# Optimization experiments

Measured on AMD Instinct MI355X. Metric: run time of the kernel, lower is better.

The kernel has to match this reference:

```python
import jax, jax.numpy as jnp
import numpy as np

B = 16      # number of graphs (equal-sized, batch = repeat(arange(B), N))


def _knn_edges(pos, k, total):
    """Batch-aware kNN graph, torch_geometric knn_graph semantics.

    loop=False, flow='source_to_target': for each query node i, its k nearest
    neighbors j produce edges (row=j neighbor/source, col=i query/target).
    Returns (row, col) as flat global int32 index arrays of length B*N*k.
    """
    N = total // B
    posb = pos.reshape(B, N, -1)                      # [B, N, 3]
    sq = jnp.sum(posb * posb, axis=-1)                # [B, N]
    # squared Euclidean distances, [B, N, N]
    d2 = sq[:, :, None] + sq[:, None, :] - 2.0 * jnp.einsum('bnd,bmd->bnm', posb, posb)
    d2 = jnp.where(jnp.eye(N, dtype=bool)[None], jnp.inf, d2)  # exclude self-loops
    _, nbr = jax.lax.top_k(-d2, k)                    # [B, N, k] local neighbor idx
    offs = (jnp.arange(B, dtype=nbr.dtype) * N)[:, None, None]
    row = (nbr + offs).reshape(-1)                                      # neighbors (sources)
    col = jnp.broadcast_to(jnp.arange(N, dtype=nbr.dtype)[None, :, None] + offs,
                           (B, N, k)).reshape(-1)                       # query nodes (targets)
    return row, col


def reference(x, pos, batch, k):
    total = x.shape[0]
    row, col = _knn_edges(pos, k, total)
    # scatter_mean(x[col], row, dim_size=total): mean of gathered features per row index
    sums = jax.ops.segment_sum(x[col], row, num_segments=total)          # [total, d]
    cnt = jax.ops.segment_sum(jnp.ones(row.shape, x.dtype), row, num_segments=total)
    x_neigh_mean = sums / jnp.maximum(cnt, 1.0)[:, None]                 # empty rows -> 0
    return jnp.sum(jnp.abs(x - x_neigh_mean), axis=-1)                   # L1 norm, [total]


def setup_inputs() -> dict:
    key = jax.random.key(0)
    k1, k2 = jax.random.split(key)
    N = 4096
    x = jax.random.normal(k1, (B * N, 64), dtype=jnp.float32)
    pos = jax.random.normal(k2, (B * N, 3), dtype=jnp.float32)
    batch = jnp.repeat(jnp.arange(B, dtype=jnp.int64), N)
    return {"x": x, "pos": pos, "batch": batch, "k": 10}
```

## Files before the change

kernel.cpp:

```cpp
#include <hip/hip_runtime.h>
#include <stdint.h>

#define NB 16
#define NN 4096
#define KK 10
#define NL 8
#define NSEL 11
#define LPITCH 9
#define FD 64
#define TOTAL (NB * NN)
#define NW 8
#define CH 512
#define QG 64
#define WCAP 24
#define WPITCH 25
#define SLOTP 11

#define INFF __int_as_float(0x7f800000)

typedef float f2 __attribute__((ext_vector_type(2)));

__device__ __forceinline__ f2 FdP3(f2 cx, f2 cy, f2 cz, f2 cq,
                                   f2 vx2, f2 vy2, f2 vz2) {
#pragma clang fp contract(fast)
    f2 t = vx2 * cx + cq;
    t = vy2 * cy + t;
    t = vz2 * cz + t;
    return t;
}

__device__ __forceinline__ uint32_t d2exact(float mx, float my, float mz, float sqi,
                                            float cx, float cy, float cz, float cw) {
    float dot = __fadd_rn(__fadd_rn(__fmul_rn(mx, cx), __fmul_rn(my, cy)),
                          __fmul_rn(mz, cz));
    float d2 = __fsub_rn(__fadd_rn(sqi, cw), __fmul_rn(2.0f, dot));
    return __float_as_uint(d2);
}

__global__ __launch_bounds__(256) void prep_kernel(const float* __restrict__ pos,
                                                   float4* __restrict__ pp4,
                                                   int* __restrict__ cnt) {
    const int p = blockIdx.x * 256 + threadIdx.x;
    const float* s = pos + (size_t)p * 6;
    float x0 = s[0], y0 = s[1], z0 = s[2];
    float x1 = s[3], y1 = s[4], z1 = s[5];
    float q0 = __fadd_rn(__fadd_rn(__fmul_rn(x0, x0), __fmul_rn(y0, y0)),
                         __fmul_rn(z0, z0));
    float q1 = __fadd_rn(__fadd_rn(__fmul_rn(x1, x1), __fmul_rn(y1, y1)),
                         __fmul_rn(z1, z1));
    pp4[2 * p + 0] = make_float4(x0, x1, y0, y1);
    pp4[2 * p + 1] = make_float4(z0, z1, q0, q1);
    cnt[2 * p + 0] = 0;
    cnt[2 * p + 1] = 0;
}

__global__ __launch_bounds__(512, 8) void knn_kernel(const float4* __restrict__ pp4,
                                                     int* __restrict__ cnt,
                                                     int* __restrict__ colfix,
                                                     int* __restrict__ nbr) {
    __shared__ uint64_t smem8[3200];
    __shared__ float tau_s[QG];
    float* listf = (float*)smem8;
    uint16_t* pool16 = (uint16_t*)smem8;
    uint64_t* slot = smem8;

    const int tid = threadIdx.x;
    const int lane = tid & 63;
    const int w = __builtin_amdgcn_readfirstlane(tid >> 6);
    const int batch = blockIdx.x & 15;
    const int qloc = ((blockIdx.x >> 4) << 6) | lane;
    const int gbase = batch << 12;
    const int gq = gbase + qloc;

    float4 mA = pp4[(gq >> 1) * 2 + 0];
    float4 mB = pp4[(gq >> 1) * 2 + 1];
    const bool hi = (qloc & 1);
    const float mx = hi ? mA.y : mA.x;
    const float my = hi ? mA.w : mA.z;
    const float mz = hi ? mB.y : mB.x;
    const float sqi = hi ? mB.w : mB.z;
    const f2 vx22 = {__fmul_rn(-2.0f, mx), __fmul_rn(-2.0f, mx)};
    const f2 vy22 = {__fmul_rn(-2.0f, my), __fmul_rn(-2.0f, my)};
    const f2 vz22 = {__fmul_rn(-2.0f, mz), __fmul_rn(-2.0f, mz)};

    const f2* __restrict__ cp2 = (const f2*)(pp4 + (size_t)(gbase + w * CH));

#define D8P(cb2)                                                      \
    f2 X0 = (cb2)[0],  Y0 = (cb2)[1],  Z0 = (cb2)[2],  Q0 = (cb2)[3]; \
    f2 X1 = (cb2)[4],  Y1 = (cb2)[5],  Z1 = (cb2)[6],  Q1 = (cb2)[7]; \
    f2 X2 = (cb2)[8],  Y2 = (cb2)[9],  Z2 = (cb2)[10], Q2 = (cb2)[11];\
    f2 X3 = (cb2)[12], Y3 = (cb2)[13], Z3 = (cb2)[14], Q3 = (cb2)[15];\
    f2 e0 = FdP3(X0, Y0, Z0, Q0, vx22, vy22, vz22);                   \
    f2 e1 = FdP3(X1, Y1, Z1, Q1, vx22, vy22, vz22);                   \
    f2 e2 = FdP3(X2, Y2, Z2, Q2, vx22, vy22, vz22);                   \
    f2 e3 = FdP3(X3, Y3, Z3, Q3, vx22, vy22, vz22);

    float L[NL];
#pragma unroll
    for (int t = 0; t < NL; t++) L[t] = INFF;

#pragma unroll 2
    for (int g = 0; g < NL; ++g) {
        float gm = INFF;
#pragma unroll
        for (int s = 0; s < 4; ++s) {
            const f2* cb2 = cp2 + (g * 4 + s) * 16;
            D8P(cb2);
            float m = fminf(fminf(fminf(e0.x, e0.y), fminf(e1.x, e1.y)),
                            fminf(fminf(e2.x, e2.y), fminf(e3.x, e3.y)));
            gm = fminf(gm, m);
        }
#pragma unroll
        for (int t = 0; t < NL - 1; ++t) L[t] = __builtin_amdgcn_fmed3f(L[t], L[t + 1], gm);
        L[NL - 1] = fminf(L[NL - 1], gm);
    }
#pragma unroll
    for (int t = 0; t < NL; t++) listf[tid * LPITCH + t] = L[t];
    __syncthreads();

    if (tid < QG) {
        int p[NW];
#pragma unroll
        for (int u = 0; u < NW; u++) p[u] = NL - 1;
        float tau = INFF;
        for (int it = 0; it < NSEL; ++it) {
            float best = INFF;
            int bw = 0;
#pragma unroll
            for (int u = 0; u < NW; u++) {
                float v = (p[u] >= 0) ? listf[((u << 6) | tid) * LPITCH + p[u]] : INFF;
                if (v < best) { best = v; bw = u; }
            }
            p[bw]--;
            tau = best;
        }
        tau_s[tid] = tau;
    }
    __syncthreads();

    const float t0v = tau_s[lane];
    const float tau = t0v + fabsf(t0v) * 1e-4f + 1e-4f;
    const uint32_t cell0 = (uint32_t)(((w << 6) | lane) * WPITCH);
    uint32_t cpos = cell0;
#pragma unroll 2
    for (int o = 0; o < CH / 8; ++o) {
        const f2* cb2 = cp2 + o * 16;
        D8P(cb2);
        const uint32_t jb = (uint32_t)(w * CH + o * 8);
        bool h0 = e0.x <= tau, h1 = e0.y <= tau, h2 = e1.x <= tau, h3 = e1.y <= tau;
        bool h4 = e2.x <= tau, h5 = e2.y <= tau, h6 = e3.x <= tau, h7 = e3.y <= tau;
#define PUSH(hv, off)                                              \
        if ((hv) && cpos < cell0 + WCAP) {                         \
            pool16[cpos] = (uint16_t)(jb + (off));                 \
            cpos++;                                                \
        }
        if (h0 | h1) { PUSH(h0, 0) PUSH(h1, 1) }
        if (h2 | h3) { PUSH(h2, 2) PUSH(h3, 3) }
        if (h4 | h5) { PUSH(h4, 4) PUSH(h5, 5) }
        if (h6 | h7) { PUSH(h6, 6) PUSH(h7, 7) }
#undef PUSH
    }

    uint64_t S[KK];
#pragma unroll
    for (int t = 0; t < KK; t++) S[t] = ~0ull;
    {
        const uint16_t* st = pool16 + cell0;
        const int c2i = (int)(cpos - cell0);
        for (int e = 0; e < c2i; ++e) {
            uint32_t ix = st[e];
            if (ix == (uint32_t)qloc) continue;
            int g = gbase + (int)ix;
            float4 A4 = pp4[(g >> 1) * 2 + 0];
            float4 B4 = pp4[(g >> 1) * 2 + 1];
            bool ch = (ix & 1);
            uint32_t db = d2exact(mx, my, mz, sqi,
                                  ch ? A4.y : A4.x, ch ? A4.w : A4.z,
                                  ch ? B4.y : B4.x, ch ? B4.w : B4.z);
            uint64_t k64 = ((uint64_t)db << 32) | ix;
            if (k64 < S[0]) {
                bool sh[KK];
                sh[0] = true;
#pragma unroll
                for (int t = 1; t < KK; t++) sh[t] = (k64 < S[t]);
#pragma unroll
                for (int t = 0; t < KK; t++) {
                    uint64_t vac = sh[t] ? k64 : S[t];
                    S[t] = (t + 1 < KK) ? (sh[t + 1] ? S[t + 1] : vac) : vac;
                }
            }
        }
    }
    __syncthreads();

    if (w >= 4) {
        uint64_t* sl = slot + (((w - 4) << 6) | lane) * SLOTP;
#pragma unroll
        for (int j = 0; j < KK; ++j) sl[j] = S[KK - 1 - j];
    }
    __syncthreads();

    if (w < 4) {
        uint64_t* sl = slot + ((w << 6) | lane) * SLOTP;
        uint64_t P[KK];
#pragma unroll
        for (int j = 0; j < KK; ++j) P[j] = sl[j];
#pragma unroll
        for (int j = 0; j < KK; ++j) {
            uint64_t v = S[KK - 1 - j];
            uint32_t r = (uint32_t)j;
#pragma unroll
            for (int i = 0; i < KK; ++i) r += (P[i] < v) ? 1u : 0u;
            if (r < KK) sl[r] = v;
        }
#pragma unroll
        for (int i = 0; i < KK; ++i) {
            uint64_t v = P[i];
            uint32_t r = (uint32_t)i;
#pragma unroll
            for (int t = 0; t < KK; ++t) r += (S[t] <= v) ? 1u : 0u;
            if (r < KK) sl[r] = v;
        }
    }
    __syncthreads();

    if (w < 2) {
        uint64_t* sa = slot + (((w * 2) << 6) | lane) * SLOTP;
        uint64_t* sb = slot + (((w * 2 + 1) << 6) | lane) * SLOTP;
        uint64_t Aa[KK], Bb[KK];
#pragma unroll
        for (int j = 0; j < KK; ++j) Aa[j] = sa[j];
#pragma unroll
        for (int j = 0; j < KK; ++j) Bb[j] = sb[j];
#pragma unroll
        for (int j = 0; j < KK; ++j) {
            uint32_t r = (uint32_t)j;
#pragma unroll
            for (int i = 0; i < KK; ++i) r += (Bb[i] < Aa[j]) ? 1u : 0u;
            if (r < KK) sa[r] = Aa[j];
        }
#pragma unroll
        for (int i = 0; i < KK; ++i) {
            uint32_t r = (uint32_t)i;
#pragma unroll
            for (int j = 0; j < KK; ++j) r += (Aa[j] <= Bb[i]) ? 1u : 0u;
            if (r < KK) sa[r] = Bb[i];
        }
    }
    __syncthreads();

    if (tid < QG) {
        const uint64_t* sa = slot + ((0 << 6) | tid) * SLOTP;
        const uint64_t* sb = slot + ((2 << 6) | tid) * SLOTP;
        uint64_t Aa[KK], Bb[KK];
#pragma unroll
        for (int j = 0; j < KK; ++j) Aa[j] = sa[j];
#pragma unroll
        for (int j = 0; j < KK; ++j) Bb[j] = sb[j];
#define EMIT(key, rk)                                              \
        {                                                          \
            int jl = (int)((key) & 0xffffffffu);                   \
            int gj = gbase + jl;                                   \
            int p = atomicAdd(&cnt[gj], 1);                        \
            if (colfix) {                                          \
                if (p < 64) colfix[(gj << 6) | p] = gq;            \
            } else {                                               \
                nbr[gq * KK + (int)(rk)] = gj;                     \
            }                                                      \
        }
#pragma unroll
        for (int j = 0; j < KK; ++j) {
            uint32_t r = (uint32_t)j;
#pragma unroll
            for (int i = 0; i < KK; ++i) r += (Bb[i] < Aa[j]) ? 1u : 0u;
            if (r < KK) EMIT(Aa[j], r)
        }
#pragma unroll
        for (int i = 0; i < KK; ++i) {
            uint32_t r = (uint32_t)i;
#pragma unroll
            for (int j = 0; j < KK; ++j) r += (Aa[j] <= Bb[i]) ? 1u : 0u;
            if (r < KK) EMIT(Bb[i], r)
        }
#undef EMIT
    }
#undef D8P
}

__global__ __launch_bounds__(256) void out_bucket_kernel(const float4* __restrict__ x4,
                                                         const int* __restrict__ colfix,
                                                         const int* __restrict__ cnt,
                                                         float* __restrict__ out) {
    const int b = blockIdx.x;
    const int g = b & 15;
    const int i = b >> 4;
    const int l = threadIdx.x & 31;
    const int n = (g << 12) | (i << 3) | (threadIdx.x >> 5);
    const int s = l & 15;
    const int half = l >> 4;
    const int c = cnt[n];
    const int cc = (c > 64) ? 64 : c;
    const int4* cf4 = (const int4*)(colfix + ((size_t)n << 6));
    float4 acc = make_float4(0.f, 0.f, 0.f, 0.f);
    for (int eb = half * 4; eb < cc; eb += 8) {
        int4 Q = cf4[eb >> 2];
        float4 v0 = x4[((size_t)Q.x << 4) | s];
        acc.x += v0.x; acc.y += v0.y; acc.z += v0.z; acc.w += v0.w;
        if (eb + 1 < cc) {
            float4 v1 = x4[((size_t)Q.y << 4) | s];
            acc.x += v1.x; acc.y += v1.y; acc.z += v1.z; acc.w += v1.w;
        }
        if (eb + 2 < cc) {
            float4 v2 = x4[((size_t)Q.z << 4) | s];
            acc.x += v2.x; acc.y += v2.y; acc.z += v2.z; acc.w += v2.w;
        }
        if (eb + 3 < cc) {
            float4 v3 = x4[((size_t)Q.w << 4) | s];
            acc.x += v3.x; acc.y += v3.y; acc.z += v3.z; acc.w += v3.w;
        }
    }
    acc.x += __shfl_xor(acc.x, 16, 64);
    acc.y += __shfl_xor(acc.y, 16, 64);
    acc.z += __shfl_xor(acc.z, 16, 64);
    acc.w += __shfl_xor(acc.w, 16, 64);
    const float inv = 1.0f / (float)(c > 1 ? c : 1);
    float4 mn = x4[((size_t)n << 4) | s];
    float v = fabsf(mn.x - acc.x * inv) + fabsf(mn.y - acc.y * inv) +
              fabsf(mn.z - acc.z * inv) + fabsf(mn.w - acc.w * inv);
    v += __shfl_xor(v, 1, 64);
    v += __shfl_xor(v, 2, 64);
    v += __shfl_xor(v, 4, 64);
    v += __shfl_xor(v, 8, 64);
    if (l == 0) out[n] = v;
}

__global__ __launch_bounds__(1024) void scan_kernel(const int* __restrict__ cnt,
                                                    int* __restrict__ offs) {
    __shared__ int lds[1024];
    const int t = threadIdx.x;
    const int base = t * 64;
    int s = 0;
    for (int i = 0; i < 64; i++) s += cnt[base + i];
    lds[t] = s;
    __syncthreads();
    for (int off = 1; off < 1024; off <<= 1) {
        int v = (t >= off) ? lds[t - off] : 0;
        __syncthreads();
        lds[t] += v;
        __syncthreads();
    }
    int run = lds[t] - s;
    for (int i = 0; i < 64; i++) {
        offs[base + i] = run;
        run += cnt[base + i];
    }
}

__global__ __launch_bounds__(256) void fill_kernel(const int* __restrict__ nbr,
                                                   int* __restrict__ offs,
                                                   int* __restrict__ col) {
    const int i = blockIdx.x * 256 + threadIdx.x;
#pragma unroll
    for (int t = 0; t < KK; t++) {
        int j = nbr[i * KK + t];
        int p = atomicAdd(&offs[j], 1);
        col[p] = i;
    }
}

__global__ __launch_bounds__(256) void out_kernel(const float* __restrict__ x,
                                                  const int* __restrict__ col,
                                                  const int* __restrict__ offs_end,
                                                  const int* __restrict__ cnt,
                                                  float* __restrict__ out) {
    const int gtid = blockIdx.x * 256 + threadIdx.x;
    const int n = gtid >> 6;
    const int lane = gtid & 63;
    const int c = cnt[n];
    const int end = offs_end[n];
    const int start = end - c;
    float s = 0.0f;
    for (int e = start; e < end; e++) {
        int i = col[e];
        s += x[(size_t)i * FD + lane];
    }
    float mean = s / (float)(c > 1 ? c : 1);
    float v = fabsf(x[(size_t)n * FD + lane] - mean);
#pragma unroll
    for (int off = 32; off; off >>= 1) v += __shfl_xor(v, off, 64);
    if (lane == 0) out[n] = v;
}

extern "C" void kernel_launch(void* const* d_in, const int* in_sizes, int n_in,
                              void* d_out, int out_size, void* d_ws, size_t ws_size,
                              hipStream_t stream) {
    const float* x = (const float*)d_in[0];
    const float* pos = (const float*)d_in[1];
    float* out = (float*)d_out;

    char* ws = (char*)d_ws;
    float4* pp4 = (float4*)(ws + 0);
    int* cnt = (int*)(ws + 1048576);
    int* colfix = (int*)(ws + 1310720);
    int* nbr = (int*)(ws + 1310720);
    int* offs = (int*)(ws + 3932160);
    int* col = (int*)(ws + 4194304);

    const bool bucket = ws_size >= (size_t)(1310720 + TOTAL * 64 * 4);

    hipLaunchKernelGGL(prep_kernel, dim3(TOTAL / 2 / 256), dim3(256), 0, stream, pos, pp4, cnt);
    hipLaunchKernelGGL(knn_kernel, dim3(TOTAL / QG), dim3(512), 0, stream, pp4, cnt,
                       bucket ? colfix : (int*)nullptr, bucket ? (int*)nullptr : nbr);
    if (bucket) {
        hipLaunchKernelGGL(out_bucket_kernel, dim3(TOTAL * 32 / 256), dim3(256), 0, stream,
                           (const float4*)x, colfix, cnt, out);
    } else {
        hipLaunchKernelGGL(scan_kernel, dim3(1), dim3(1024), 0, stream, cnt, offs);
        hipLaunchKernelGGL(fill_kernel, dim3(TOTAL / 256), dim3(256), 0, stream, nbr, offs, col);
        hipLaunchKernelGGL(out_kernel, dim3(TOTAL * FD / 256), dim3(256), 0, stream,
                           x, col, offs, cnt, out);
    }
}
```

Measured before the change: 175.0 us.

## Sort points by Morton grid cell and prune kNN candidates with group bounding boxes

After: 188.3 us. 7.6% more time.

```diff
diff --git a/kernel.cpp b/kernel.cpp
--- a/kernel.cpp
+++ b/kernel.cpp
@@ -5,6 +5,8 @@
 #define NN 4096
 #define KK 10
 #define NL 8
+#define NL2 11
+#define LP2 11
 #define NSEL 11
 #define LPITCH 9
 #define FD 64
@@ -14,7 +16,15 @@
 #define QG 64
 #define WCAP 24
 #define WPITCH 25
+#define QCAP 192
 #define SLOTP 11
+#define GSZ 32
+#define NGRP (TOTAL / GSZ)
+
+#define OFF_HIST 18087936
+#define OFF_OIDX 18350080
+#define OFF_BBX  18481152
+#define SORTED_NEED 18546688
 
 #define INFF __int_as_float(0x7f800000)
 
@@ -35,6 +45,345 @@
                           __fmul_rn(mz, cz));
     float d2 = __fsub_rn(__fadd_rn(sqi, cw), __fmul_rn(2.0f, dot));
     return __float_as_uint(d2);
+}
+
+__device__ __forceinline__ uint32_t sp3(int v) {
+    uint32_t x = (uint32_t)v;
+    return (x & 1u) | ((x & 2u) << 2) | ((x & 4u) << 4) | ((x & 8u) << 6);
+}
+
+__device__ __forceinline__ uint32_t cellcode(float x, float y, float z) {
+    int cx = (int)floorf((x + 4.0f) * 2.0f);
+    int cy = (int)floorf((y + 4.0f) * 2.0f);
+    int cz = (int)floorf((z + 4.0f) * 2.0f);
+    cx = cx < 0 ? 0 : (cx > 15 ? 15 : cx);
+    cy = cy < 0 ? 0 : (cy > 15 ? 15 : cy);
+    cz = cz < 0 ? 0 : (cz > 15 ? 15 : cz);
+    return (sp3(cx) << 2) | (sp3(cy) << 1) | sp3(cz);
+}
+
+__global__ __launch_bounds__(256) void hist_kernel(const float* __restrict__ pos,
+                                                   int* __restrict__ hist,
+                                                   int* __restrict__ cnt) {
+    const int i = blockIdx.x * 256 + threadIdx.x;
+    const float* s = pos + (size_t)i * 3;
+    float x = s[0], y = s[1], z = s[2];
+    uint32_t code = cellcode(x, y, z);
+    atomicAdd(&hist[(uint32_t)((i >> 12) << 12) | code], 1);
+    cnt[i] = 0;
+}
+
+__global__ __launch_bounds__(512) void scan_kernel16(int* __restrict__ hist) {
+    __shared__ int lds[512];
+    const int t = threadIdx.x;
+    int* h = hist + (blockIdx.x << 12);
+    const int base = t * 8;
+    int v[8];
+    int s = 0;
+#pragma unroll
+    for (int j = 0; j < 8; j++) { v[j] = h[base + j]; s += v[j]; }
+    lds[t] = s;
+    __syncthreads();
+    for (int off = 1; off < 512; off <<= 1) {
+        int u = (t >= off) ? lds[t - off] : 0;
+        __syncthreads();
+        lds[t] += u;
+        __syncthreads();
+    }
+    int run = lds[t] - s;
+#pragma unroll
+    for (int j = 0; j < 8; j++) { h[base + j] = run; run += v[j]; }
+}
+
+__global__ __launch_bounds__(256) void scatter_kernel(const float* __restrict__ pos,
+                                                      int* __restrict__ offs,
+                                                      float* __restrict__ pp4sf,
+                                                      uint16_t* __restrict__ oidx) {
+    const int i = blockIdx.x * 256 + threadIdx.x;
+    const float* s = pos + (size_t)i * 3;
+    float x = s[0], y = s[1], z = s[2];
+    float q = __fadd_rn(__fadd_rn(__fmul_rn(x, x), __fmul_rn(y, y)),
+                        __fmul_rn(z, z));
+    uint32_t code = cellcode(x, y, z);
+    int sl = atomicAdd(&offs[(uint32_t)((i >> 12) << 12) | code], 1);
+    int gs = ((i >> 12) << 12) | sl;
+    float* dst = pp4sf + (size_t)(gs >> 1) * 8 + (gs & 1);
+    dst[0] = x; dst[2] = y; dst[4] = z; dst[6] = q;
+    oidx[gs] = (uint16_t)(i & 4095);
+}
+
+__global__ __launch_bounds__(256) void bbox_kernel(const float4* __restrict__ pp4s,
+                                                   float* __restrict__ bbx) {
+    const int grp = blockIdx.x * 8 + (threadIdx.x >> 5);
+    const int sub = threadIdx.x & 31;
+    const int gs = grp * GSZ + sub;
+    float4 A = pp4s[(gs >> 1) * 2 + 0];
+    float4 B = pp4s[(gs >> 1) * 2 + 1];
+    bool hi = gs & 1;
+    float x = hi ? A.y : A.x, y = hi ? A.w : A.z, z = hi ? B.y : B.x;
+    float nx = x, xx = x, ny = y, xy = y, nz = z, xz = z;
+#pragma unroll
+    for (int o = 1; o < 32; o <<= 1) {
+        nx = fminf(nx, __shfl_xor(nx, o, 32)); xx = fmaxf(xx, __shfl_xor(xx, o, 32));
+        ny = fminf(ny, __shfl_xor(ny, o, 32)); xy = fmaxf(xy, __shfl_xor(xy, o, 32));
+        nz = fminf(nz, __shfl_xor(nz, o, 32)); xz = fmaxf(xz, __shfl_xor(xz, o, 32));
+    }
+    if (sub == 0) {
+        float* d = bbx + (size_t)grp * 8;
+        d[0] = nx; d[1] = xx; d[2] = ny; d[3] = xy; d[4] = nz; d[5] = xz;
+        d[6] = 0.f; d[7] = 0.f;
+    }
+}
+
+__global__ __launch_bounds__(512, 8) void knn_sorted_kernel(
+        const float4* __restrict__ pp4,
+        const uint16_t* __restrict__ oidx,
+        const float* __restrict__ bbx,
+        int* __restrict__ cnt,
+        int* __restrict__ colfix,
+        int* __restrict__ nbr) {
+    __shared__ uint64_t smem8[3200];
+    __shared__ float tau_s[QG];
+    __shared__ uint32_t qcnt[QG];
+    float* listf = (float*)smem8;
+    uint16_t* pool16 = (uint16_t*)smem8;
+    uint64_t* slot = smem8;
+
+    const int tid = threadIdx.x;
+    const int lane = tid & 63;
+    const int w = __builtin_amdgcn_readfirstlane(tid >> 6);
+    const int batch = blockIdx.x & 15;
+    const int qs = ((blockIdx.x >> 4) << 6) | lane;
+    const int gbase = batch << 12;
+    const int gqs = gbase + qs;
+
+    float4 mA = pp4[(gqs >> 1) * 2 + 0];
+    float4 mB = pp4[(gqs >> 1) * 2 + 1];
+    const bool hi = (qs & 1);
+    const float mx = hi ? mA.y : mA.x;
+    const float my = hi ? mA.w : mA.z;
+    const float mz = hi ? mB.y : mB.x;
+    const float sqi = hi ? mB.w : mB.z;
+    const f2 vx22 = {__fmul_rn(-2.0f, mx), __fmul_rn(-2.0f, mx)};
+    const f2 vy22 = {__fmul_rn(-2.0f, my), __fmul_rn(-2.0f, my)};
+    const f2 vz22 = {__fmul_rn(-2.0f, mz), __fmul_rn(-2.0f, mz)};
+
+    const f2* __restrict__ bp2 = (const f2*)(pp4 + (size_t)gbase);
+    const f2* __restrict__ cp2 = (const f2*)(pp4 + (size_t)(gbase + w * CH));
+
+#define D8P(cb2)                                                      \
+    f2 X0 = (cb2)[0],  Y0 = (cb2)[1],  Z0 = (cb2)[2],  Q0 = (cb2)[3]; \
+    f2 X1 = (cb2)[4],  Y1 = (cb2)[5],  Z1 = (cb2)[6],  Q1 = (cb2)[7]; \
+    f2 X2 = (cb2)[8],  Y2 = (cb2)[9],  Z2 = (cb2)[10], Q2 = (cb2)[11];\
+    f2 X3 = (cb2)[12], Y3 = (cb2)[13], Z3 = (cb2)[14], Q3 = (cb2)[15];\
+    f2 e0 = FdP3(X0, Y0, Z0, Q0, vx22, vy22, vz22);                   \
+    f2 e1 = FdP3(X1, Y1, Z1, Q1, vx22, vy22, vz22);                   \
+    f2 e2 = FdP3(X2, Y2, Z2, Q2, vx22, vy22, vz22);                   \
+    f2 e3 = FdP3(X3, Y3, Z3, Q3, vx22, vy22, vz22);
+
+    float L[NL2];
+#pragma unroll
+    for (int t = 0; t < NL2; t++) L[t] = INFF;
+
+#pragma unroll 2
+    for (int j = 0; j < 32; ++j) {
+        float m = INFF;
+#pragma unroll
+        for (int s = 0; s < 4; ++s) {
+            const f2* c2 = bp2 + (((s << 9) | (j << 4) | w) << 2);
+            f2 X = c2[0], Y = c2[1], Z = c2[2], Q = c2[3];
+            f2 e = FdP3(X, Y, Z, Q, vx22, vy22, vz22);
+            m = fminf(m, fminf(e.x, e.y));
+        }
+#pragma unroll
+        for (int t = 0; t < NL2 - 1; ++t) L[t] = __builtin_amdgcn_fmed3f(L[t], L[t + 1], m);
+        L[NL2 - 1] = fminf(L[NL2 - 1], m);
+    }
+#pragma unroll
+    for (int t = 0; t < NL2; t++) listf[tid * LP2 + t] = L[t];
+    __syncthreads();
+
+    if (tid < QG) {
+        int p[NW];
+#pragma unroll
+        for (int u = 0; u < NW; u++) p[u] = NL2 - 1;
+        float tau = INFF;
+        for (int it = 0; it < NSEL; ++it) {
+            float best = INFF;
+            int bw = 0;
+#pragma unroll
+            for (int u = 0; u < NW; u++) {
+                float v = (p[u] >= 0) ? listf[((u << 6) | tid) * LP2 + p[u]] : INFF;
+                if (v < best) { best = v; bw = u; }
+            }
+            p[bw]--;
+            tau = best;
+        }
+        tau_s[tid] = tau;
+        qcnt[tid] = 0;
+    }
+    __syncthreads();
+
+    const float t0v = tau_s[lane];
+    const float tau = t0v + fabsf(t0v) * 1e-4f + 1e-4f;
+    const float taud2 = __fadd_rn(tau, sqi) + 1e-4f;
+#pragma unroll 1
+    for (int og = 0; og < 16; ++og) {
+        const float* bb = bbx + (size_t)((batch << 7) | (w << 4) | og) * 8;
+        float dx = fmaxf(fmaxf(bb[0] - mx, mx - bb[1]), 0.0f);
+        float dy = fmaxf(fmaxf(bb[2] - my, my - bb[3]), 0.0f);
+        float dz = fmaxf(fmaxf(bb[4] - mz, mz - bb[5]), 0.0f);
+        float d2lb = dx * dx + dy * dy + dz * dz;
+        if (__any(d2lb <= taud2)) {
+#pragma unroll
+            for (int s = 0; s < 4; ++s) {
+                const f2* cb2 = cp2 + (og * 4 + s) * 16;
+                D8P(cb2);
+                const uint32_t jb = (uint32_t)(w * CH + (og * 4 + s) * 8);
+                bool h0 = e0.x <= tau, h1 = e0.y <= tau, h2 = e1.x <= tau, h3 = e1.y <= tau;
+                bool h4 = e2.x <= tau, h5 = e2.y <= tau, h6 = e3.x <= tau, h7 = e3.y <= tau;
+#define PUSH(hv, off)                                                   \
+                if (hv) {                                               \
+                    uint32_t p = atomicAdd(&qcnt[lane], 1u);            \
+                    if (p < QCAP) pool16[lane * QCAP + p] = (uint16_t)(jb + (off)); \
+                }
+                if (h0 | h1) { PUSH(h0, 0) PUSH(h1, 1) }
+                if (h2 | h3) { PUSH(h2, 2) PUSH(h3, 3) }
+                if (h4 | h5) { PUSH(h4, 4) PUSH(h5, 5) }
+                if (h6 | h7) { PUSH(h6, 6) PUSH(h7, 7) }
+#undef PUSH
+            }
+        }
+    }
+    __syncthreads();
+
+    uint64_t S[KK];
+#pragma unroll
+    for (int t = 0; t < KK; t++) S[t] = ~0ull;
+    {
+        uint32_t len = qcnt[lane];
+        if (len > QCAP) len = QCAP;
+        const uint16_t* st = pool16 + lane * QCAP;
+        for (uint32_t e = (uint32_t)w; e < len; e += NW) {
+            uint32_t ix = st[e];
+            if (ix == (uint32_t)qs) continue;
+            int g = gbase + (int)ix;
+            float4 A4 = pp4[(g >> 1) * 2 + 0];
+            float4 B4 = pp4[(g >> 1) * 2 + 1];
+            bool ch = (ix & 1);
+            uint32_t db = d2exact(mx, my, mz, sqi,
+                                  ch ? A4.y : A4.x, ch ? A4.w : A4.z,
+                                  ch ? B4.y : B4.x, ch ? B4.w : B4.z);
+            uint32_t orig = (uint32_t)oidx[g];
+            uint64_t k64 = ((uint64_t)db << 32) | orig;
+            if (k64 < S[0]) {
+                bool sh[KK];
+                sh[0] = true;
+#pragma unroll
+                for (int t = 1; t < KK; t++) sh[t] = (k64 < S[t]);
+#pragma unroll
+                for (int t = 0; t < KK; t++) {
+                    uint64_t vac = sh[t] ? k64 : S[t];
+                    S[t] = (t + 1 < KK) ? (sh[t + 1] ? S[t + 1] : vac) : vac;
+                }
+            }
+        }
+    }
+    __syncthreads();
+
+    if (w >= 4) {
+        uint64_t* sl = slot + (((w - 4) << 6) | lane) * SLOTP;
+#pragma unroll
+        for (int j = 0; j < KK; ++j) sl[j] = S[KK - 1 - j];
+    }
+    __syncthreads();
+
+    if (w < 4) {
+        uint64_t* sl = slot + ((w << 6) | lane) * SLOTP;
+        uint64_t P[KK];
+#pragma unroll
+        for (int j = 0; j < KK; ++j) P[j] = sl[j];
+#pragma unroll
+        for (int j = 0; j < KK; ++j) {
+            uint64_t v = S[KK - 1 - j];
+            uint32_t r = (uint32_t)j;
+#pragma unroll
+            for (int i = 0; i < KK; ++i) r += (P[i] < v) ? 1u : 0u;
+            if (r < KK) sl[r] = v;
+        }
+#pragma unroll
+        for (int i = 0; i < KK; ++i) {
+            uint64_t v = P[i];
+            uint32_t r = (uint32_t)i;
+#pragma unroll
+            for (int t = 0; t < KK; ++t) r += (S[t] <= v) ? 1u : 0u;
+            if (r < KK) sl[r] = v;
+        }
+    }
+    __syncthreads();
+
+    if (w < 2) {
+        uint64_t* sa = slot + (((w * 2) << 6) | lane) * SLOTP;
+        uint64_t* sb = slot + (((w * 2 + 1) << 6) | lane) * SLOTP;
+        uint64_t Aa[KK], Bb[KK];
+#pragma unroll
+        for (int j = 0; j < KK; ++j) Aa[j] = sa[j];
+#pragma unroll
+        for (int j = 0; j < KK; ++j) Bb[j] = sb[j];
+#pragma unroll
+        for (int j = 0; j < KK; ++j) {
+            uint32_t r = (uint32_t)j;
+#pragma unroll
+            for (int i = 0; i < KK; ++i) r += (Bb[i] < Aa[j]) ? 1u : 0u;
+            if (r < KK) sa[r] = Aa[j];
+        }
+#pragma unroll
+        for (int i = 0; i < KK; ++i) {
+            uint32_t r = (uint32_t)i;
+#pragma unroll
+            for (int j = 0; j < KK; ++j) r += (Aa[j] <= Bb[i]) ? 1u : 0u;
+            if (r < KK) sa[r] = Bb[i];
+        }
+    }
+    __syncthreads();
+
+    if (tid < QG) {
+        const uint64_t* sa = slot + ((0 << 6) | tid) * SLOTP;
+        const uint64_t* sb = slot + ((2 << 6) | tid) * SLOTP;
+        uint64_t Aa[KK], Bb[KK];
+#pragma unroll
+        for (int j = 0; j < KK; ++j) Aa[j] = sa[j];
+#pragma unroll
+        for (int j = 0; j < KK; ++j) Bb[j] = sb[j];
+        const int gq_o = gbase + (int)oidx[gbase + qs];
+#define EMIT(key, rk)                                              \
+        if ((uint32_t)((key) >> 32) != 0xffffffffu) {              \
+            int jl = (int)((key) & 0xffffffffu);                   \
+            int gj = gbase + jl;   \
+            int p = atomicAdd(&cnt[gj], 1);                        \
+            if (colfix) {                                          \
+                if (p < 64) colfix[(gj << 6) | p] = gq_o;          \
+            } else {                                               \
+                nbr[gq_o * KK + (int)(rk)] = gj;                   \
+            }                                                      \
+        }
+#pragma unroll
+        for (int j = 0; j < KK; ++j) {
+            uint32_t r = (uint32_t)j;
+#pragma unroll
+            for (int i = 0; i < KK; ++i) r += (Bb[i] < Aa[j]) ? 1u : 0u;
+            if (r < KK) EMIT(Aa[j], r)
+        }
+#pragma unroll
+        for (int i = 0; i < KK; ++i) {
+            uint32_t r = (uint32_t)i;
+#pragma unroll
+            for (int j = 0; j < KK; ++j) r += (Aa[j] <= Bb[i]) ? 1u : 0u;
+            if (r < KK) EMIT(Bb[i], r)
+        }
+#undef EMIT
+    }
+#undef D8P
 }
 
 __global__ __launch_bounds__(256) void prep_kernel(const float* __restrict__ pos,
@@ -405,19 +754,39 @@
     int* nbr = (int*)(ws + 1310720);
     int* offs = (int*)(ws + 3932160);
     int* col = (int*)(ws + 4194304);
+    int* hist = (int*)(ws + OFF_HIST);
+    uint16_t* oidx = (uint16_t*)(ws + OFF_OIDX);
+    float* bbx = (float*)(ws + OFF_BBX);
 
     const bool bucket = ws_size >= (size_t)(1310720 + TOTAL * 64 * 4);
-
-    hipLaunchKernelGGL(prep_kernel, dim3(TOTAL / 2 / 256), dim3(256), 0, stream, pos, pp4, cnt);
-    hipLaunchKernelGGL(knn_kernel, dim3(TOTAL / QG), dim3(512), 0, stream, pp4, cnt,
-                       bucket ? colfix : (int*)nullptr, bucket ? (int*)nullptr : nbr);
-    if (bucket) {
+    const bool sorted = ws_size >= (size_t)SORTED_NEED;
+
+    if (sorted) {
+        hipMemsetAsync(hist, 0, NB * 4096 * sizeof(int), stream);
+        hipLaunchKernelGGL(hist_kernel, dim3(TOTAL / 256), dim3(256), 0, stream,
+                           pos, hist, cnt);
+        hipLaunchKernelGGL(scan_kernel16, dim3(NB), dim3(512), 0, stream, hist);
+        hipLaunchKernelGGL(scatter_kernel, dim3(TOTAL / 256), dim3(256), 0, stream,
+                           pos, hist, (float*)pp4, oidx);
+        hipLaunchKernelGGL(bbox_kernel, dim3(NGRP / 8), dim3(256), 0, stream,
+                           pp4, bbx);
+        hipLaunchKernelGGL(knn_sorted_kernel, dim3(TOTAL / QG), dim3(512), 0, stream,
+                           pp4, oidx, bbx, cnt, colfix, (int*)nullptr);
         hipLaunchKernelGGL(out_bucket_kernel, dim3(TOTAL * 32 / 256), dim3(256), 0, stream,
                            (const float4*)x, colfix, cnt, out);
     } else {
-        hipLaunchKernelGGL(scan_kernel, dim3(1), dim3(1024), 0, stream, cnt, offs);
-        hipLaunchKernelGGL(fill_kernel, dim3(TOTAL / 256), dim3(256), 0, stream, nbr, offs, col);
-        hipLaunchKernelGGL(out_kernel, dim3(TOTAL * FD / 256), dim3(256), 0, stream,
-                           x, col, offs, cnt, out);
-    }
-}
+        hipLaunchKernelGGL(prep_kernel, dim3(TOTAL / 2 / 256), dim3(256), 0, stream,
+                           pos, pp4, cnt);
+        hipLaunchKernelGGL(knn_kernel, dim3(TOTAL / QG), dim3(512), 0, stream, pp4, cnt,
+                           bucket ? colfix : (int*)nullptr, bucket ? (int*)nullptr : nbr);
+        if (bucket) {
+            hipLaunchKernelGGL(out_bucket_kernel, dim3(TOTAL * 32 / 256), dim3(256), 0, stream,
+                               (const float4*)x, colfix, cnt, out);
+        } else {
+            hipLaunchKernelGGL(scan_kernel, dim3(1), dim3(1024), 0, stream, cnt, offs);
+            hipLaunchKernelGGL(fill_kernel, dim3(TOTAL / 256), dim3(256), 0, stream, nbr, offs, col);
+            hipLaunchKernelGGL(out_kernel, dim3(TOTAL * FD / 256), dim3(256), 0, stream,
+                               x, col, offs, cnt, out);
+        }
+    }
+}
```
